# Kernel optimization log

Hardware: AMD Instinct MI355X
Metric: run time of the kernel (lower is better)

## Reference

```python
import jax, jax.numpy as jnp
import numpy as np

EMBED = 256
HEADS = 8
LEVELS = 4
POINTS = 4
HD = EMBED // HEADS  # 32


def _bilinear_sample(v, grid):
    """torch.F.grid_sample(mode='bilinear', padding_mode='zeros', align_corners=False).
    v: (B, C, H, W); grid: (B, Q, P, 2) with xy coords in [-1, 1].
    Returns (B, C, Q, P).
    """
    B, C, H, W = v.shape
    x = (grid[..., 0] + 1.0) * (W * 0.5) - 0.5
    y = (grid[..., 1] + 1.0) * (H * 0.5) - 0.5
    x0f = jnp.floor(x)
    y0f = jnp.floor(y)
    wx = x - x0f
    wy = y - y0f
    x0 = x0f.astype(jnp.int32)
    y0 = y0f.astype(jnp.int32)
    vf = v.reshape(B, C, H * W)

    def corner(xi, yi, w):
        valid = (xi >= 0) & (xi < W) & (yi >= 0) & (yi < H)
        idx = jnp.clip(yi, 0, H - 1) * W + jnp.clip(xi, 0, W - 1)  # (B, Q, P)
        g = jax.vmap(lambda vb, ib: jnp.take(vb, ib, axis=1))(vf, idx.reshape(B, -1))
        g = g.reshape(B, C, idx.shape[1], idx.shape[2])  # (B, C, Q, P)
        return g * (w * valid.astype(v.dtype))[:, None]

    return (corner(x0, y0, (1 - wx) * (1 - wy))
            + corner(x0 + 1, y0, wx * (1 - wy))
            + corner(x0, y0 + 1, (1 - wx) * wy)
            + corner(x0 + 1, y0 + 1, wx * wy))


def setup_inputs() -> dict:
    key = jax.random.key(0)
    ks = jax.random.split(key, 16)
    N, Q, D = 2, 8192, EMBED
    inp = {
        'query': jax.random.normal(ks[0], (N, Q, D), jnp.float32),
        'feat0': jax.random.normal(ks[1], (N, D, 64, 64), jnp.float32),
        'feat1': jax.random.normal(ks[2], (N, D, 32, 32), jnp.float32),
        'feat2': jax.random.normal(ks[3], (N, D, 16, 16), jnp.float32),
        'feat3': jax.random.normal(ks[4], (N, D, 8, 8), jnp.float32),
        'reference_points': jax.random.uniform(ks[5], (N, Q, 2), jnp.float32),
        # params stored as (in, out); equivalent math to torch Linear's x @ W.T + b
        'W_off': jax.random.normal(ks[6], (D, HEADS * LEVELS * POINTS * 2), jnp.float32) * 0.01,
        'b_off': jax.random.normal(ks[7], (HEADS * LEVELS * POINTS * 2,), jnp.float32) * 0.01,
        'W_attn': jax.random.normal(ks[8], (D, HEADS * LEVELS * POINTS), jnp.float32) * 0.02,
        'b_attn': jax.random.normal(ks[9], (HEADS * LEVELS * POINTS,), jnp.float32) * 0.02,
        'W_val': jax.random.normal(ks[10], (D, D), jnp.float32) * (1.0 / np.sqrt(D)),
        'b_val': jnp.zeros((D,), jnp.float32),
        'W_out': jax.random.normal(ks[11], (D, D), jnp.float32) * (1.0 / np.sqrt(D)),
        'b_out': jnp.zeros((D,), jnp.float32),
    }
    return inp


def reference(query, feat0, feat1, feat2, feat3, reference_points,
              W_off, b_off, W_attn, b_attn, W_val, b_val, W_out, b_out):
    feats = [feat0, feat1, feat2, feat3]
    N, Q, D = query.shape
    # offset / attention-weight projections
    off = (query @ W_off + b_off).reshape(N, Q, HEADS, LEVELS, POINTS, 2)
    attn = (query @ W_attn + b_attn).reshape(N, Q, HEADS, LEVELS, POINTS)
    # reference points (N,Q,2) -> (N,Q,L,2)
    ref = jnp.broadcast_to(reference_points[:, :, None, :], (N, Q, LEVELS, 2))
    # value projection (1x1 conv) per level, split heads -> (N*H, hd, H_l, W_l)
    vals = [(jnp.einsum('bchw,cd->bdhw', f, W_val) + b_val[None, :, None, None])
            .reshape(N * HEADS, HD, f.shape[2], f.shape[3]) for f in feats]
    # flatten batch*heads
    off = off.transpose(0, 2, 1, 3, 4, 5).reshape(N * HEADS, Q, LEVELS, POINTS, 2)
    attn = attn.transpose(0, 2, 1, 3, 4).reshape(N * HEADS, Q, LEVELS, POINTS)
    refh = jnp.broadcast_to(ref[:, None], (N, HEADS, Q, LEVELS, 2)).reshape(N * HEADS, Q, LEVELS, 2)
    loc = refh[:, :, :, None, :] + off                 # (NH, Q, L, P, 2) in [0,1]
    grid = 2.0 * loc - 1.0                             # [-1, 1]
    # per-level bilinear sampling -> (NH, hd, Q, L, P)
    sampled = jnp.stack([_bilinear_sample(vals[l], grid[:, :, l]) for l in range(LEVELS)], axis=-2)
    # softmax over levels*points
    aw = jax.nn.softmax(attn.reshape(N * HEADS, Q, LEVELS * POINTS), axis=-1)
    aw = jnp.nan_to_num(aw).reshape(N * HEADS, Q, LEVELS, POINTS)
    out = jnp.einsum('bcqlp,bqlp->bcq', sampled, aw)   # (NH, hd, Q)
    out = out.reshape(N, HEADS, HD, Q).transpose(0, 3, 1, 2).reshape(N, Q, D)
    return out @ W_out + b_out
```

## Files before the change

kernel.cpp:

```cpp
#include <hip/hip_runtime.h>
#include <math.h>

#define NB 2
#define QN 8192
#define DIM 256
#define S_TOT 5440

typedef unsigned int uint32;
typedef _Float16 f16;
typedef __attribute__((ext_vector_type(8))) _Float16 h8;
typedef __attribute__((ext_vector_type(2))) _Float16 h2;
typedef __attribute__((ext_vector_type(4))) float f32x4;
typedef __attribute__((ext_vector_type(4))) uint32 u32x4;

__global__ __launch_bounds__(256) void prep_kernel(
    const float* __restrict__ f0, const float* __restrict__ f1,
    const float* __restrict__ f2, const float* __restrict__ f3,
    const float* __restrict__ W_off, const float* __restrict__ W_attn,
    const float* __restrict__ W_val, const float* __restrict__ W_out,
    f16* __restrict__ featT, f16* __restrict__ Wcat_t,
    f16* __restrict__ Wval_t, f16* __restrict__ Wout_t) {
  const int t = blockIdx.x;
  const float* src;
  f16* dst;
  int S, tb;
  if (t < 340) {
    const int b = (t >= 170) ? 1 : 0;
    const int tt = t - 170 * b;
    int soff;
    if (tt < 128)      { src = f0; S = 4096; soff = 0;    tb = tt; }
    else if (tt < 160) { src = f1; S = 1024; soff = 4096; tb = tt - 128; }
    else if (tt < 168) { src = f2; S = 256;  soff = 5120; tb = tt - 160; }
    else               { src = f3; S = 64;   soff = 5376; tb = tt - 168; }
    src += (size_t)b * 256 * S;
    dst = featT + ((size_t)b * S_TOT + soff) * 256;
  } else {
    const int tw = t - 340;
    if (tw < 8)       { src = W_off;  dst = Wcat_t;             S = 256; tb = tw; }
    else if (tw < 12) { src = W_attn; dst = Wcat_t + 256 * 256; S = 128; tb = tw - 8; }
    else if (tw < 20) { src = W_val;  dst = Wval_t;             S = 256; tb = tw - 12; }
    else              { src = W_out;  dst = Wout_t;             S = 256; tb = tw - 20; }
  }
  const int s0 = tb * 32, c0 = blockIdx.y * 32;

  __shared__ float tile[32][33];
  const int tx = threadIdx.x & 31, ty = threadIdx.x >> 5;
#pragma unroll
  for (int j = 0; j < 4; ++j) {
    const int c = c0 + ty + j * 8;
    tile[ty + j * 8][tx] = src[(size_t)c * S + s0 + tx];
  }
  __syncthreads();
#pragma unroll
  for (int j = 0; j < 4; ++j) {
    const int srow = s0 + ty + j * 8;
    dst[(size_t)srow * 256 + c0 + tx] = (f16)tile[tx][ty + j * 8];
  }
}

__global__ __launch_bounds__(256) void gemm_fused_kernel(
    const f16* __restrict__ featT, const float* __restrict__ query,
    const f16* __restrict__ Wval_t, const f16* __restrict__ Wcat_t,
    const float* __restrict__ b_val, const float* __restrict__ b_off,
    const float* __restrict__ b_attn,
    f16* __restrict__ vals, f16* __restrict__ offb, f16* __restrict__ attnb) {
  __shared__ f16 As[64][256];
  __shared__ f16 Bs[64][256];
  const int t = blockIdx.x;
  const int tid = threadIdx.x;
  const bool isval = (t < 680);
  size_t r0, c0;
  const f16* Bt;
  if (isval) { r0 = (size_t)(t >> 2) * 64;      c0 = (size_t)(t & 3) * 64;  Bt = Wval_t; }
  else       { const int t2 = t - 680;
               r0 = (size_t)(t2 / 6) * 64;      c0 = (size_t)(t2 % 6) * 64; Bt = Wcat_t; }

  {
    const f16* gb = Bt + c0 * 256;
    const int row = tid >> 5, slot = tid & 31;
#pragma unroll
    for (int i = 0; i < 8; ++i) {
      const int r = i * 8 + row;
      const int ph = (slot & 24) | ((slot ^ r) & 7);
      if (isval) {
        *(u32x4*)&As[r][ph * 8] =
            *(const u32x4*)(featT + (r0 + r) * 256 + slot * 8);
      } else {
        const float* ga = query + (r0 + r) * 256 + slot * 8;
        const float4 u0 = *(const float4*)ga;
        const float4 u1 = *(const float4*)(ga + 4);
        h8 hv = {(f16)u0.x, (f16)u0.y, (f16)u0.z, (f16)u0.w,
                 (f16)u1.x, (f16)u1.y, (f16)u1.z, (f16)u1.w};
        *(h8*)&As[r][ph * 8] = hv;
      }
      *(u32x4*)&Bs[r][ph * 8] = *(const u32x4*)(gb + (size_t)r * 256 + slot * 8);
    }
  }
  __syncthreads();

  const int wid = tid >> 6, lane = tid & 63;
  const int wr = (wid >> 1) * 32, wc = (wid & 1) * 32;
  const int l15 = lane & 15, l4 = lane >> 4;

  f32x4 acc[2][2] = {};
#pragma unroll
  for (int ks = 0; ks < 8; ++ks) {
    const int slot = ks * 4 + l4;
    h8 a[2], b[2];
#pragma unroll
    for (int m = 0; m < 2; ++m) {
      const int r = wr + m * 16 + l15;
      const int ph = (slot & 24) | ((slot ^ r) & 7);
      a[m] = *(const h8*)&As[r][ph * 8];
    }
#pragma unroll
    for (int n = 0; n < 2; ++n) {
      const int r = wc + n * 16 + l15;
      const int ph = (slot & 24) | ((slot ^ r) & 7);
      b[n] = *(const h8*)&Bs[r][ph * 8];
    }
#pragma unroll
    for (int m = 0; m < 2; ++m)
#pragma unroll
      for (int n = 0; n < 2; ++n)
        acc[m][n] = __builtin_amdgcn_mfma_f32_16x16x32_f16(a[m], b[n], acc[m][n], 0, 0, 0);
  }

#pragma unroll
  for (int m = 0; m < 2; ++m)
#pragma unroll
    for (int n = 0; n < 2; ++n)
#pragma unroll
      for (int r = 0; r < 4; ++r) {
        const size_t row = r0 + wr + m * 16 + l4 * 4 + r;
        const size_t col = c0 + wc + n * 16 + l15;
        const float v = acc[m][n][r];
        if (isval) {
          vals[row * 256 + col] = (f16)(v + b_val[col]);
        } else if (c0 < 256) {
          offb[row * 256 + col] = (f16)(v + b_off[col]);
        } else {
          attnb[row * 128 + (col - 256)] = (f16)(v + b_attn[col - 256]);
        }
      }
}

__global__ __launch_bounds__(256) void gemm_out_kernel(
    const f16* __restrict__ A, const f16* __restrict__ Bt,
    const float* __restrict__ bias, float* __restrict__ out) {
  __shared__ f16 As[64][256];
  __shared__ f16 Bs[64][256];
  const int tid = threadIdx.x;
  const size_t r0 = (size_t)blockIdx.x * 64;
  const size_t c0 = (size_t)blockIdx.y * 64;

  {
    const f16* ga = A + r0 * 256;
    const f16* gb = Bt + c0 * 256;
    const int row = tid >> 5, slot = tid & 31;
#pragma unroll
    for (int i = 0; i < 8; ++i) {
      const int r = i * 8 + row;
      const int ph = (slot & 24) | ((slot ^ r) & 7);
      *(u32x4*)&As[r][ph * 8] = *(const u32x4*)(ga + (size_t)r * 256 + slot * 8);
      *(u32x4*)&Bs[r][ph * 8] = *(const u32x4*)(gb + (size_t)r * 256 + slot * 8);
    }
  }
  __syncthreads();

  const int wid = tid >> 6, lane = tid & 63;
  const int wr = (wid >> 1) * 32, wc = (wid & 1) * 32;
  const int l15 = lane & 15, l4 = lane >> 4;

  f32x4 acc[2][2] = {};
#pragma unroll
  for (int ks = 0; ks < 8; ++ks) {
    const int slot = ks * 4 + l4;
    h8 a[2], b[2];
#pragma unroll
    for (int m = 0; m < 2; ++m) {
      const int r = wr + m * 16 + l15;
      const int ph = (slot & 24) | ((slot ^ r) & 7);
      a[m] = *(const h8*)&As[r][ph * 8];
    }
#pragma unroll
    for (int n = 0; n < 2; ++n) {
      const int r = wc + n * 16 + l15;
      const int ph = (slot & 24) | ((slot ^ r) & 7);
      b[n] = *(const h8*)&Bs[r][ph * 8];
    }
#pragma unroll
    for (int m = 0; m < 2; ++m)
#pragma unroll
      for (int n = 0; n < 2; ++n)
        acc[m][n] = __builtin_amdgcn_mfma_f32_16x16x32_f16(a[m], b[n], acc[m][n], 0, 0, 0);
  }

#pragma unroll
  for (int m = 0; m < 2; ++m)
#pragma unroll
    for (int n = 0; n < 2; ++n)
#pragma unroll
      for (int r = 0; r < 4; ++r) {
        const size_t row = r0 + wr + m * 16 + l4 * 4 + r;
        const size_t col = c0 + wc + n * 16 + l15;
        out[row * 256 + col] = acc[m][n][r] + bias[col];
      }
}

__global__ __launch_bounds__(256) void sample_kernel(
    const f16* __restrict__ vals, const f16* __restrict__ offb,
    const f16* __restrict__ attnb, const float* __restrict__ refp,
    f16* __restrict__ samp) {
  const int tid = threadIdx.x;
  const int g = tid & 15;
  const int grp = tid >> 4;
  const int h = grp & 7;
  const int half = tid >> 7;
  const int bq = blockIdx.x * 2 + half;
  const int b = bq >> 13;

  __shared__ float4 wts[16][17];
  __shared__ int4 idxs[16][17];

  const float rx = refp[(size_t)bq * 2 + 0];
  const float ry = refp[(size_t)bq * 2 + 1];

  float logit = (float)attnb[(size_t)bq * 128 + h * 16 + g];
  float m = logit;
#pragma unroll
  for (int mask = 1; mask < 16; mask <<= 1)
    m = fmaxf(m, __shfl_xor(m, mask, 16));
  const float e = __expf(logit - m);
  float ssum = e;
#pragma unroll
  for (int mask = 1; mask < 16; mask <<= 1)
    ssum += __shfl_xor(ssum, mask, 16);
  const float aw = e / ssum;

  const h2 ov = *(const h2*)(offb + (size_t)bq * 256 + h * 32 + g * 2);
  const int l = g >> 2;
  const int Wl = 64 >> l;
  const int loff = (l == 0) ? 0 : (l == 1) ? 4096 : (l == 2) ? 5120 : 5376;

  const float px = (rx + (float)ov[0]) * (float)Wl - 0.5f;
  const float py = (ry + (float)ov[1]) * (float)Wl - 0.5f;
  const float fx = floorf(px), fy = floorf(py);
  const float wx = px - fx, wy = py - fy;
  const int x0 = (int)fx, y0 = (int)fy;
  const int x1 = x0 + 1, y1 = y0 + 1;
  const float vx0 = (x0 >= 0 && x0 < Wl) ? 1.f : 0.f;
  const float vx1 = (x1 >= 0 && x1 < Wl) ? 1.f : 0.f;
  const float vy0 = (y0 >= 0 && y0 < Wl) ? 1.f : 0.f;
  const float vy1 = (y1 >= 0 && y1 < Wl) ? 1.f : 0.f;
  const int cx0 = min(max(x0, 0), Wl - 1), cx1 = min(max(x1, 0), Wl - 1);
  const int cy0 = min(max(y0, 0), Wl - 1), cy1 = min(max(y1, 0), Wl - 1);
  const int base = b * S_TOT + loff;
  idxs[grp][g] = make_int4((base + cy0 * Wl + cx0) * 512,
                           (base + cy0 * Wl + cx1) * 512,
                           (base + cy1 * Wl + cx0) * 512,
                           (base + cy1 * Wl + cx1) * 512);
  wts[grp][g] = make_float4(aw * (1.f - wx) * (1.f - wy) * vx0 * vy0,
                            aw * wx * (1.f - wy) * vx1 * vy0,
                            aw * (1.f - wx) * wy * vx0 * vy1,
                            aw * wx * wy * vx1 * vy1);
  __syncthreads();

  const int c4 = g & 3, pc = g >> 2;
  const char* vb = (const char*)vals + (h * 64 + c4 * 16);

  float wv[16];
  int ids[16];
#pragma unroll
  for (int pt = 0; pt < 16; ++pt) {
    wv[pt] = ((const float*)&wts[grp][pt])[pc];
    ids[pt] = ((const int*)&idxs[grp][pt])[pc];
  }
  h8 vv[16];
#pragma unroll
  for (int pt = 0; pt < 16; ++pt) vv[pt] = *(const h8*)(vb + ids[pt]);

  float a[8] = {};
#pragma unroll
  for (int pt = 0; pt < 16; ++pt) {
#pragma unroll
    for (int k = 0; k < 8; ++k) a[k] = fmaf((float)vv[pt][k], wv[pt], a[k]);
  }
#pragma unroll
  for (int k = 0; k < 8; ++k) {
    a[k] += __shfl_xor(a[k], 4);
    a[k] += __shfl_xor(a[k], 8);
  }
  if (pc == 0) {
    h8 r;
#pragma unroll
    for (int k = 0; k < 8; ++k) r[k] = (f16)a[k];
    *(h8*)(samp + (size_t)bq * 256 + h * 32 + c4 * 8) = r;
  }
}

extern "C" void kernel_launch(void* const* d_in, const int* in_sizes, int n_in,
                              void* d_out, int out_size, void* d_ws, size_t ws_size,
                              hipStream_t stream) {
  const float* query = (const float*)d_in[0];
  const float* feat[4] = {(const float*)d_in[1], (const float*)d_in[2],
                          (const float*)d_in[3], (const float*)d_in[4]};
  const float* refp  = (const float*)d_in[5];
  const float* W_off = (const float*)d_in[6];
  const float* b_off = (const float*)d_in[7];
  const float* W_attn = (const float*)d_in[8];
  const float* b_attn = (const float*)d_in[9];
  const float* W_val = (const float*)d_in[10];
  const float* b_val = (const float*)d_in[11];
  const float* W_out = (const float*)d_in[12];
  const float* b_out = (const float*)d_in[13];
  float* out = (float*)d_out;

  f16* ws = (f16*)d_ws;
  f16* featT  = ws;
  f16* vals   = featT + (size_t)NB * S_TOT * 256;
  f16* offb   = vals + (size_t)NB * S_TOT * 256;
  f16* samp   = offb + (size_t)NB * QN * 256;
  f16* attnb  = samp + (size_t)NB * QN * 256;
  f16* Wcat_t = attnb + (size_t)NB * QN * 128;
  f16* Wval_t = Wcat_t + 384 * 256;
  f16* Wout_t = Wval_t + 256 * 256;

  prep_kernel<<<dim3(368, 8), 256, 0, stream>>>(
      feat[0], feat[1], feat[2], feat[3], W_off, W_attn, W_val, W_out,
      featT, Wcat_t, Wval_t, Wout_t);

  gemm_fused_kernel<<<680 + 1536, 256, 0, stream>>>(
      featT, query, Wval_t, Wcat_t, b_val, b_off, b_attn, vals, offb, attnb);

  sample_kernel<<<(NB * QN) / 2, 256, 0, stream>>>(vals, offb, attnb, refp, samp);

  gemm_out_kernel<<<dim3((NB * QN) / 64, 4), 256, 0, stream>>>(
      samp, Wout_t, b_out, out);
}
```

Before: 80.98 us.

## Loop over column tiles per block reusing A tile with B register prefetch

Both GEMM kernels now assign one 64-row strip per block and iterate over all 64-column output tiles. The A tile is loaded (and for query, converted to fp16) once and cached in registers, and the next B tile is prefetched into registers while the current one is used. This removes redundant A loads and conversions across column-tile blocks. In exchange it cuts the grid size by 4-6x, reducing parallelism and raising register pressure.

```diff
diff --git a/kernel.cpp b/kernel.cpp
--- a/kernel.cpp
+++ b/kernel.cpp
@@ -68,81 +68,103 @@
   __shared__ f16 Bs[64][256];
   const int t = blockIdx.x;
   const int tid = threadIdx.x;
-  const bool isval = (t < 680);
-  size_t r0, c0;
-  const f16* Bt;
-  if (isval) { r0 = (size_t)(t >> 2) * 64;      c0 = (size_t)(t & 3) * 64;  Bt = Wval_t; }
-  else       { const int t2 = t - 680;
-               r0 = (size_t)(t2 / 6) * 64;      c0 = (size_t)(t2 % 6) * 64; Bt = Wcat_t; }
-
-  {
-    const f16* gb = Bt + c0 * 256;
-    const int row = tid >> 5, slot = tid & 31;
+  const bool isval = (t < 170);
+  const size_t r0 = (size_t)(isval ? t : t - 170) * 64;
+  const int NC = isval ? 4 : 6;
+  const f16* Bt = isval ? Wval_t : Wcat_t;
+
+  const int row = tid >> 5, slot = tid & 31;
+
+#pragma unroll
+  for (int i = 0; i < 8; ++i) {
+    const int r = i * 8 + row;
+    const int ph = (slot & 24) | ((slot ^ r) & 7);
+    if (isval) {
+      *(u32x4*)&As[r][ph * 8] =
+          *(const u32x4*)(featT + (r0 + r) * 256 + slot * 8);
+    } else {
+      const float* ga = query + (r0 + r) * 256 + slot * 8;
+      const float4 u0 = *(const float4*)ga;
+      const float4 u1 = *(const float4*)(ga + 4);
+      h8 hv = {(f16)u0.x, (f16)u0.y, (f16)u0.z, (f16)u0.w,
+               (f16)u1.x, (f16)u1.y, (f16)u1.z, (f16)u1.w};
+      *(h8*)&As[r][ph * 8] = hv;
+    }
+  }
+
+  const int wid = tid >> 6, lane = tid & 63;
+  const int wr = (wid >> 1) * 32, wc = (wid & 1) * 32;
+  const int l15 = lane & 15, l4 = lane >> 4;
+
+  u32x4 bpre[8];
+#pragma unroll
+  for (int i = 0; i < 8; ++i) {
+    bpre[i] = *(const u32x4*)(Bt + (size_t)(i * 8 + row) * 256 + slot * 8);
+  }
+
+  h8 areg[8][2];
+
+  for (int c = 0; c < NC; ++c) {
+    __syncthreads();
 #pragma unroll
     for (int i = 0; i < 8; ++i) {
       const int r = i * 8 + row;
       const int ph = (slot & 24) | ((slot ^ r) & 7);
-      if (isval) {
-        *(u32x4*)&As[r][ph * 8] =
-            *(const u32x4*)(featT + (r0 + r) * 256 + slot * 8);
-      } else {
-        const float* ga = query + (r0 + r) * 256 + slot * 8;
-        const float4 u0 = *(const float4*)ga;
-        const float4 u1 = *(const float4*)(ga + 4);
-        h8 hv = {(f16)u0.x, (f16)u0.y, (f16)u0.z, (f16)u0.w,
-                 (f16)u1.x, (f16)u1.y, (f16)u1.z, (f16)u1.w};
-        *(h8*)&As[r][ph * 8] = hv;
-      }
-      *(u32x4*)&Bs[r][ph * 8] = *(const u32x4*)(gb + (size_t)r * 256 + slot * 8);
-    }
-  }
-  __syncthreads();
-
-  const int wid = tid >> 6, lane = tid & 63;
-  const int wr = (wid >> 1) * 32, wc = (wid & 1) * 32;
-  const int l15 = lane & 15, l4 = lane >> 4;
-
-  f32x4 acc[2][2] = {};
-#pragma unroll
-  for (int ks = 0; ks < 8; ++ks) {
-    const int slot = ks * 4 + l4;
-    h8 a[2], b[2];
-#pragma unroll
-    for (int m = 0; m < 2; ++m) {
-      const int r = wr + m * 16 + l15;
-      const int ph = (slot & 24) | ((slot ^ r) & 7);
-      a[m] = *(const h8*)&As[r][ph * 8];
-    }
-#pragma unroll
-    for (int n = 0; n < 2; ++n) {
-      const int r = wc + n * 16 + l15;
-      const int ph = (slot & 24) | ((slot ^ r) & 7);
-      b[n] = *(const h8*)&Bs[r][ph * 8];
-    }
+      *(u32x4*)&Bs[r][ph * 8] = bpre[i];
+    }
+    __syncthreads();
+
+    if (c + 1 < NC) {
+#pragma unroll
+      for (int i = 0; i < 8; ++i) {
+        bpre[i] = *(const u32x4*)(Bt + (size_t)((c + 1) * 64 + i * 8 + row) * 256 + slot * 8);
+      }
+    }
+
+    f32x4 acc[2][2] = {};
+#pragma unroll
+    for (int ks = 0; ks < 8; ++ks) {
+      const int slot2 = ks * 4 + l4;
+      if (c == 0) {
+#pragma unroll
+        for (int m = 0; m < 2; ++m) {
+          const int r = wr + m * 16 + l15;
+          const int ph = (slot2 & 24) | ((slot2 ^ r) & 7);
+          areg[ks][m] = *(const h8*)&As[r][ph * 8];
+        }
+      }
+      h8 b[2];
+#pragma unroll
+      for (int n = 0; n < 2; ++n) {
+        const int r = wc + n * 16 + l15;
+        const int ph = (slot2 & 24) | ((slot2 ^ r) & 7);
+        b[n] = *(const h8*)&Bs[r][ph * 8];
+      }
+#pragma unroll
+      for (int m = 0; m < 2; ++m)
+#pragma unroll
+        for (int n = 0; n < 2; ++n)
+          acc[m][n] = __builtin_amdgcn_mfma_f32_16x16x32_f16(areg[ks][m], b[n], acc[m][n], 0, 0, 0);
+    }
+
 #pragma unroll
     for (int m = 0; m < 2; ++m)
 #pragma unroll
       for (int n = 0; n < 2; ++n)
-        acc[m][n] = __builtin_amdgcn_mfma_f32_16x16x32_f16(a[m], b[n], acc[m][n], 0, 0, 0);
-  }
-
-#pragma unroll
-  for (int m = 0; m < 2; ++m)
-#pragma unroll
-    for (int n = 0; n < 2; ++n)
-#pragma unroll
-      for (int r = 0; r < 4; ++r) {
-        const size_t row = r0 + wr + m * 16 + l4 * 4 + r;
-        const size_t col = c0 + wc + n * 16 + l15;
-        const float v = acc[m][n][r];
-        if (isval) {
-          vals[row * 256 + col] = (f16)(v + b_val[col]);
-        } else if (c0 < 256) {
-          offb[row * 256 + col] = (f16)(v + b_off[col]);
-        } else {
-          attnb[row * 128 + (col - 256)] = (f16)(v + b_attn[col - 256]);
+#pragma unroll
+        for (int r = 0; r < 4; ++r) {
+          const size_t rw = r0 + wr + m * 16 + l4 * 4 + r;
+          const int col = c * 64 + wc + n * 16 + l15;
+          const float v = acc[m][n][r];
+          if (isval) {
+            vals[rw * 256 + col] = (f16)(v + b_val[col]);
+          } else if (col < 256) {
+            offb[rw * 256 + col] = (f16)(v + b_off[col]);
+          } else {
+            attnb[rw * 128 + (col - 256)] = (f16)(v + b_attn[col - 256]);
+          }
         }
-      }
+  }
 }
 
 __global__ __launch_bounds__(256) void gemm_out_kernel(
@@ -152,60 +174,81 @@
   __shared__ f16 Bs[64][256];
   const int tid = threadIdx.x;
   const size_t r0 = (size_t)blockIdx.x * 64;
-  const size_t c0 = (size_t)blockIdx.y * 64;
-
-  {
-    const f16* ga = A + r0 * 256;
-    const f16* gb = Bt + c0 * 256;
-    const int row = tid >> 5, slot = tid & 31;
+
+  const int row = tid >> 5, slot = tid & 31;
+#pragma unroll
+  for (int i = 0; i < 8; ++i) {
+    const int r = i * 8 + row;
+    const int ph = (slot & 24) | ((slot ^ r) & 7);
+    *(u32x4*)&As[r][ph * 8] = *(const u32x4*)(A + (r0 + r) * 256 + slot * 8);
+  }
+
+  const int wid = tid >> 6, lane = tid & 63;
+  const int wr = (wid >> 1) * 32, wc = (wid & 1) * 32;
+  const int l15 = lane & 15, l4 = lane >> 4;
+
+  u32x4 bpre[8];
+#pragma unroll
+  for (int i = 0; i < 8; ++i) {
+    bpre[i] = *(const u32x4*)(Bt + (size_t)(i * 8 + row) * 256 + slot * 8);
+  }
+
+  h8 areg[8][2];
+
+  for (int c = 0; c < 4; ++c) {
+    __syncthreads();
 #pragma unroll
     for (int i = 0; i < 8; ++i) {
       const int r = i * 8 + row;
       const int ph = (slot & 24) | ((slot ^ r) & 7);
-      *(u32x4*)&As[r][ph * 8] = *(const u32x4*)(ga + (size_t)r * 256 + slot * 8);
-      *(u32x4*)&Bs[r][ph * 8] = *(const u32x4*)(gb + (size_t)r * 256 + slot * 8);
-    }
-  }
-  __syncthreads();
-
-  const int wid = tid >> 6, lane = tid & 63;
-  const int wr = (wid >> 1) * 32, wc = (wid & 1) * 32;
-  const int l15 = lane & 15, l4 = lane >> 4;
-
-  f32x4 acc[2][2] = {};
-#pragma unroll
-  for (int ks = 0; ks < 8; ++ks) {
-    const int slot = ks * 4 + l4;
-    h8 a[2], b[2];
-#pragma unroll
-    for (int m = 0; m < 2; ++m) {
-      const int r = wr + m * 16 + l15;
-      const int ph = (slot & 24) | ((slot ^ r) & 7);
-      a[m] = *(const h8*)&As[r][ph * 8];
-    }
-#pragma unroll
-    for (int n = 0; n < 2; ++n) {
-      const int r = wc + n * 16 + l15;
-      const int ph = (slot & 24) | ((slot ^ r) & 7);
-      b[n] = *(const h8*)&Bs[r][ph * 8];
-    }
+      *(u32x4*)&Bs[r][ph * 8] = bpre[i];
+    }
+    __syncthreads();
+
+    if (c + 1 < 4) {
+#pragma unroll
+      for (int i = 0; i < 8; ++i) {
+        bpre[i] = *(const u32x4*)(Bt + (size_t)((c + 1) * 64 + i * 8 + row) * 256 + slot * 8);
+      }
+    }
+
+    f32x4 acc[2][2] = {};
+#pragma unroll
+    for (int ks = 0; ks < 8; ++ks) {
+      const int slot2 = ks * 4 + l4;
+      if (c == 0) {
+#pragma unroll
+        for (int m = 0; m < 2; ++m) {
+          const int r = wr + m * 16 + l15;
+          const int ph = (slot2 & 24) | ((slot2 ^ r) & 7);
+          areg[ks][m] = *(const h8*)&As[r][ph * 8];
+        }
+      }
+      h8 b[2];
+#pragma unroll
+      for (int n = 0; n < 2; ++n) {
+        const int r = wc + n * 16 + l15;
+        const int ph = (slot2 & 24) | ((slot2 ^ r) & 7);
+        b[n] = *(const h8*)&Bs[r][ph * 8];
+      }
+#pragma unroll
+      for (int m = 0; m < 2; ++m)
+#pragma unroll
+        for (int n = 0; n < 2; ++n)
+          acc[m][n] = __builtin_amdgcn_mfma_f32_16x16x32_f16(areg[ks][m], b[n], acc[m][n], 0, 0, 0);
+    }
+
 #pragma unroll
     for (int m = 0; m < 2; ++m)
 #pragma unroll
       for (int n = 0; n < 2; ++n)
-        acc[m][n] = __builtin_amdgcn_mfma_f32_16x16x32_f16(a[m], b[n], acc[m][n], 0, 0, 0);
-  }
-
-#pragma unroll
-  for (int m = 0; m < 2; ++m)
-#pragma unroll
-    for (int n = 0; n < 2; ++n)
-#pragma unroll
-      for (int r = 0; r < 4; ++r) {
-        const size_t row = r0 + wr + m * 16 + l4 * 4 + r;
-        const size_t col = c0 + wc + n * 16 + l15;
-        out[row * 256 + col] = acc[m][n][r] + bias[col];
-      }
+#pragma unroll
+        for (int r = 0; r < 4; ++r) {
+          const size_t rw = r0 + wr + m * 16 + l4 * 4 + r;
+          const int col = c * 64 + wc + n * 16 + l15;
+          out[rw * 256 + col] = acc[m][n][r] + bias[col];
+        }
+  }
 }
 
 __global__ __launch_bounds__(256) void sample_kernel(
@@ -330,11 +373,10 @@
       feat[0], feat[1], feat[2], feat[3], W_off, W_attn, W_val, W_out,
       featT, Wcat_t, Wval_t, Wout_t);
 
-  gemm_fused_kernel<<<680 + 1536, 256, 0, stream>>>(
+  gemm_fused_kernel<<<170 + 256, 256, 0, stream>>>(
       featT, query, Wval_t, Wcat_t, b_val, b_off, b_attn, vals, offb, attnb);
 
   sample_kernel<<<(NB * QN) / 2, 256, 0, stream>>>(vals, offb, attnb, refp, samp);
 
-  gemm_out_kernel<<<dim3((NB * QN) / 64, 4), 256, 0, stream>>>(
-      samp, Wout_t, b_out, out);
-}
+  gemm_out_kernel<<<(NB * QN) / 64, 256, 0, stream>>>(samp, Wout_t, b_out, out);
+}
```

Measured after the change: 69.28 us. 14.5% less time.

## Pre-swizzle GEMM operands into MFMA fragment layout and drop LDS staging

Applied to the files above, without the earlier changes.

Query, features, weights and sampled outputs are written by the producers in a blocked fragment layout (16-row groups × 8-wide K chunks), so the GEMM kernels load MFMA operands straight from global memory without shared-memory staging or barriers. Query fp32→fp16 conversion moves into the prep kernel. GEMM tiles change to 32 rows × full width per block, so each block covers all output columns and there are fewer, larger blocks. The intent is to remove LDS traffic and syncs. In exchange, weight fragments are re-read from global/L2 by every block and the query conversion becomes an extra pass through memory. The samp buffer is aliased onto qf to reuse workspace.

```diff
diff --git a/kernel.cpp b/kernel.cpp
--- a/kernel.cpp
+++ b/kernel.cpp
@@ -11,207 +11,198 @@
 typedef __attribute__((ext_vector_type(8))) _Float16 h8;
 typedef __attribute__((ext_vector_type(2))) _Float16 h2;
 typedef __attribute__((ext_vector_type(4))) float f32x4;
-typedef __attribute__((ext_vector_type(4))) uint32 u32x4;
+
 
 __global__ __launch_bounds__(256) void prep_kernel(
+    const float* __restrict__ q,
     const float* __restrict__ f0, const float* __restrict__ f1,
     const float* __restrict__ f2, const float* __restrict__ f3,
     const float* __restrict__ W_off, const float* __restrict__ W_attn,
     const float* __restrict__ W_val, const float* __restrict__ W_out,
-    f16* __restrict__ featT, f16* __restrict__ Wcat_t,
-    f16* __restrict__ Wval_t, f16* __restrict__ Wout_t) {
-  const int t = blockIdx.x;
+    f16* __restrict__ qf, f16* __restrict__ featT_f,
+    f16* __restrict__ Wcat_f, f16* __restrict__ Wval_f, f16* __restrict__ Wout_f) {
+  const int t = blockIdx.x, y = blockIdx.y, tid = threadIdx.x;
+
+  if (t < 128) {
+    const int row0 = (t * 8 + y) * 16;
+    const int s_l = tid >> 4, c8 = tid & 15;
+    const float* src = q + (size_t)(row0 + s_l) * 256;
+#pragma unroll
+    for (int cc = 0; cc < 2; ++cc) {
+      const int c8c = c8 + cc * 16;
+      const float4 u0 = *(const float4*)(src + c8c * 8);
+      const float4 u1 = *(const float4*)(src + c8c * 8 + 4);
+      h8 hv = {(f16)u0.x, (f16)u0.y, (f16)u0.z, (f16)u0.w,
+               (f16)u1.x, (f16)u1.y, (f16)u1.z, (f16)u1.w};
+      *(h8*)(qf + ((size_t)(row0 >> 4) * 32 + c8c) * 128 + s_l * 8) = hv;
+    }
+    return;
+  }
+
+  __shared__ float tile[32][33];
+  const int tx = tid & 31, ty = tid >> 5;
   const float* src;
   f16* dst;
-  int S, tb;
-  if (t < 340) {
-    const int b = (t >= 170) ? 1 : 0;
-    const int tt = t - 170 * b;
+  int S, tb, s_base = 0;
+
+  if (t < 468) {
+    const int tt0 = t - 128;
+    const int b = (tt0 >= 170) ? 1 : 0;
+    const int tt = tt0 - 170 * b;
     int soff;
     if (tt < 128)      { src = f0; S = 4096; soff = 0;    tb = tt; }
     else if (tt < 160) { src = f1; S = 1024; soff = 4096; tb = tt - 128; }
     else if (tt < 168) { src = f2; S = 256;  soff = 5120; tb = tt - 160; }
     else               { src = f3; S = 64;   soff = 5376; tb = tt - 168; }
     src += (size_t)b * 256 * S;
-    dst = featT + ((size_t)b * S_TOT + soff) * 256;
+    dst = featT_f;
+    s_base = b * S_TOT + soff;
   } else {
-    const int tw = t - 340;
-    if (tw < 8)       { src = W_off;  dst = Wcat_t;             S = 256; tb = tw; }
-    else if (tw < 12) { src = W_attn; dst = Wcat_t + 256 * 256; S = 128; tb = tw - 8; }
-    else if (tw < 20) { src = W_val;  dst = Wval_t;             S = 256; tb = tw - 12; }
-    else              { src = W_out;  dst = Wout_t;             S = 256; tb = tw - 20; }
-  }
-  const int s0 = tb * 32, c0 = blockIdx.y * 32;
-
-  __shared__ float tile[32][33];
-  const int tx = threadIdx.x & 31, ty = threadIdx.x >> 5;
+    const int tw = t - 468;
+    if (tw < 8)       { src = W_off;  dst = Wcat_f; S = 256; tb = tw;      s_base = 0; }
+    else if (tw < 12) { src = W_attn; dst = Wcat_f; S = 128; tb = tw - 8;  s_base = 256; }
+    else if (tw < 20) { src = W_val;  dst = Wval_f; S = 256; tb = tw - 12; s_base = 0; }
+    else              { src = W_out;  dst = Wout_f; S = 256; tb = tw - 20; s_base = 0; }
+  }
+  const int s0 = tb * 32, c0 = y * 32;
+
 #pragma unroll
   for (int j = 0; j < 4; ++j) {
     const int c = c0 + ty + j * 8;
     tile[ty + j * 8][tx] = src[(size_t)c * S + s0 + tx];
   }
   __syncthreads();
-#pragma unroll
-  for (int j = 0; j < 4; ++j) {
-    const int srow = s0 + ty + j * 8;
-    dst[(size_t)srow * 256 + c0 + tx] = (f16)tile[tx][ty + j * 8];
+
+  if (tid < 128) {
+    const int s_l = tid >> 2, c8l = tid & 3;
+    const int Sg = s_base + s0 + s_l;
+    const int c8 = (c0 >> 3) + c8l;
+    h8 v;
+#pragma unroll
+    for (int j = 0; j < 8; ++j) v[j] = (f16)tile[c8l * 8 + j][s_l];
+    *(h8*)(dst + ((size_t)(Sg >> 4) * 32 + c8) * 128 + (Sg & 15) * 8) = v;
   }
 }
 
 __global__ __launch_bounds__(256) void gemm_fused_kernel(
-    const f16* __restrict__ featT, const float* __restrict__ query,
-    const f16* __restrict__ Wval_t, const f16* __restrict__ Wcat_t,
+    const f16* __restrict__ qf, const f16* __restrict__ featT_f,
+    const f16* __restrict__ Wcat_f, const f16* __restrict__ Wval_f,
     const float* __restrict__ b_val, const float* __restrict__ b_off,
     const float* __restrict__ b_attn,
     f16* __restrict__ vals, f16* __restrict__ offb, f16* __restrict__ attnb) {
-  __shared__ f16 As[64][256];
-  __shared__ f16 Bs[64][256];
   const int t = blockIdx.x;
   const int tid = threadIdx.x;
-  const bool isval = (t < 680);
-  size_t r0, c0;
-  const f16* Bt;
-  if (isval) { r0 = (size_t)(t >> 2) * 64;      c0 = (size_t)(t & 3) * 64;  Bt = Wval_t; }
-  else       { const int t2 = t - 680;
-               r0 = (size_t)(t2 / 6) * 64;      c0 = (size_t)(t2 % 6) * 64; Bt = Wcat_t; }
-
-  {
-    const f16* gb = Bt + c0 * 256;
-    const int row = tid >> 5, slot = tid & 31;
-#pragma unroll
-    for (int i = 0; i < 8; ++i) {
-      const int r = i * 8 + row;
-      const int ph = (slot & 24) | ((slot ^ r) & 7);
-      if (isval) {
-        *(u32x4*)&As[r][ph * 8] =
-            *(const u32x4*)(featT + (r0 + r) * 256 + slot * 8);
-      } else {
-        const float* ga = query + (r0 + r) * 256 + slot * 8;
-        const float4 u0 = *(const float4*)ga;
-        const float4 u1 = *(const float4*)(ga + 4);
-        h8 hv = {(f16)u0.x, (f16)u0.y, (f16)u0.z, (f16)u0.w,
-                 (f16)u1.x, (f16)u1.y, (f16)u1.z, (f16)u1.w};
-        *(h8*)&As[r][ph * 8] = hv;
-      }
-      *(u32x4*)&Bs[r][ph * 8] = *(const u32x4*)(gb + (size_t)r * 256 + slot * 8);
+  const int lane = tid & 63, wid = tid >> 6;
+  const int l15 = lane & 15, l4 = lane >> 4;
+
+  if (t < 340) {
+    const int g0 = t * 2;
+    f32x4 acc[2][4] = {};
+#pragma unroll
+    for (int ks = 0; ks < 8; ++ks) {
+      const int s2 = ks * 4 + l4;
+      h8 a[2], b[4];
+#pragma unroll
+      for (int m = 0; m < 2; ++m)
+        a[m] = *(const h8*)(featT_f + ((size_t)(g0 + m) * 32 + s2) * 128 + l15 * 8);
+#pragma unroll
+      for (int n = 0; n < 4; ++n)
+        b[n] = *(const h8*)(Wval_f + ((size_t)(wid * 4 + n) * 32 + s2) * 128 + l15 * 8);
+#pragma unroll
+      for (int m = 0; m < 2; ++m)
+#pragma unroll
+        for (int n = 0; n < 4; ++n)
+          acc[m][n] = __builtin_amdgcn_mfma_f32_16x16x32_f16(a[m], b[n], acc[m][n], 0, 0, 0);
     }
-  }
-  __syncthreads();
-
-  const int wid = tid >> 6, lane = tid & 63;
-  const int wr = (wid >> 1) * 32, wc = (wid & 1) * 32;
-  const int l15 = lane & 15, l4 = lane >> 4;
-
-  f32x4 acc[2][2] = {};
-#pragma unroll
-  for (int ks = 0; ks < 8; ++ks) {
-    const int slot = ks * 4 + l4;
-    h8 a[2], b[2];
-#pragma unroll
-    for (int m = 0; m < 2; ++m) {
-      const int r = wr + m * 16 + l15;
-      const int ph = (slot & 24) | ((slot ^ r) & 7);
-      a[m] = *(const h8*)&As[r][ph * 8];
+#pragma unroll
+    for (int m = 0; m < 2; ++m)
+#pragma unroll
+      for (int n = 0; n < 4; ++n)
+#pragma unroll
+        for (int r = 0; r < 4; ++r) {
+          const size_t rw = (size_t)t * 32 + m * 16 + l4 * 4 + r;
+          const int col = wid * 64 + n * 16 + l15;
+          vals[rw * 256 + col] = (f16)(acc[m][n][r] + b_val[col]);
+        }
+  } else {
+    const int t2 = t - 340;
+    const int g0 = t2 * 2;
+    f32x4 acc[2][6] = {};
+#pragma unroll
+    for (int ks = 0; ks < 8; ++ks) {
+      const int s2 = ks * 4 + l4;
+      h8 a[2], b[6];
+#pragma unroll
+      for (int m = 0; m < 2; ++m)
+        a[m] = *(const h8*)(qf + ((size_t)(g0 + m) * 32 + s2) * 128 + l15 * 8);
+#pragma unroll
+      for (int n = 0; n < 6; ++n)
+        b[n] = *(const h8*)(Wcat_f + ((size_t)(wid * 6 + n) * 32 + s2) * 128 + l15 * 8);
+#pragma unroll
+      for (int m = 0; m < 2; ++m)
+#pragma unroll
+        for (int n = 0; n < 6; ++n)
+          acc[m][n] = __builtin_amdgcn_mfma_f32_16x16x32_f16(a[m], b[n], acc[m][n], 0, 0, 0);
     }
 #pragma unroll
-    for (int n = 0; n < 2; ++n) {
-      const int r = wc + n * 16 + l15;
-      const int ph = (slot & 24) | ((slot ^ r) & 7);
-      b[n] = *(const h8*)&Bs[r][ph * 8];
-    }
-#pragma unroll
     for (int m = 0; m < 2; ++m)
 #pragma unroll
-      for (int n = 0; n < 2; ++n)
-        acc[m][n] = __builtin_amdgcn_mfma_f32_16x16x32_f16(a[m], b[n], acc[m][n], 0, 0, 0);
-  }
-
-#pragma unroll
-  for (int m = 0; m < 2; ++m)
-#pragma unroll
-    for (int n = 0; n < 2; ++n)
-#pragma unroll
-      for (int r = 0; r < 4; ++r) {
-        const size_t row = r0 + wr + m * 16 + l4 * 4 + r;
-        const size_t col = c0 + wc + n * 16 + l15;
-        const float v = acc[m][n][r];
-        if (isval) {
-          vals[row * 256 + col] = (f16)(v + b_val[col]);
-        } else if (c0 < 256) {
-          offb[row * 256 + col] = (f16)(v + b_off[col]);
-        } else {
-          attnb[row * 128 + (col - 256)] = (f16)(v + b_attn[col - 256]);
+      for (int n = 0; n < 6; ++n)
+#pragma unroll
+        for (int r = 0; r < 4; ++r) {
+          const size_t rw = (size_t)t2 * 32 + m * 16 + l4 * 4 + r;
+          const int col = wid * 96 + n * 16 + l15;
+          const float v = acc[m][n][r];
+          if (col < 256)
+            offb[rw * 256 + col] = (f16)(v + b_off[col]);
+          else
+            attnb[rw * 128 + (col - 256)] = (f16)(v + b_attn[col - 256]);
         }
-      }
+  }
 }
 
 __global__ __launch_bounds__(256) void gemm_out_kernel(
     const f16* __restrict__ A, const f16* __restrict__ Bt,
     const float* __restrict__ bias, float* __restrict__ out) {
-  __shared__ f16 As[64][256];
-  __shared__ f16 Bs[64][256];
   const int tid = threadIdx.x;
-  const size_t r0 = (size_t)blockIdx.x * 64;
-  const size_t c0 = (size_t)blockIdx.y * 64;
-
-  {
-    const f16* ga = A + r0 * 256;
-    const f16* gb = Bt + c0 * 256;
-    const int row = tid >> 5, slot = tid & 31;
-#pragma unroll
-    for (int i = 0; i < 8; ++i) {
-      const int r = i * 8 + row;
-      const int ph = (slot & 24) | ((slot ^ r) & 7);
-      *(u32x4*)&As[r][ph * 8] = *(const u32x4*)(ga + (size_t)r * 256 + slot * 8);
-      *(u32x4*)&Bs[r][ph * 8] = *(const u32x4*)(gb + (size_t)r * 256 + slot * 8);
-    }
-  }
-  __syncthreads();
-
-  const int wid = tid >> 6, lane = tid & 63;
-  const int wr = (wid >> 1) * 32, wc = (wid & 1) * 32;
+  const int lane = tid & 63, wid = tid >> 6;
   const int l15 = lane & 15, l4 = lane >> 4;
-
-  f32x4 acc[2][2] = {};
+  const int g0 = blockIdx.x * 2;
+
+  f32x4 acc[2][4] = {};
 #pragma unroll
   for (int ks = 0; ks < 8; ++ks) {
-    const int slot = ks * 4 + l4;
-    h8 a[2], b[2];
-#pragma unroll
-    for (int m = 0; m < 2; ++m) {
-      const int r = wr + m * 16 + l15;
-      const int ph = (slot & 24) | ((slot ^ r) & 7);
-      a[m] = *(const h8*)&As[r][ph * 8];
-    }
-#pragma unroll
-    for (int n = 0; n < 2; ++n) {
-      const int r = wc + n * 16 + l15;
-      const int ph = (slot & 24) | ((slot ^ r) & 7);
-      b[n] = *(const h8*)&Bs[r][ph * 8];
-    }
+    const int s2 = ks * 4 + l4;
+    h8 a[2], b[4];
 #pragma unroll
     for (int m = 0; m < 2; ++m)
-#pragma unroll
-      for (int n = 0; n < 2; ++n)
+      a[m] = *(const h8*)(A + ((size_t)(g0 + m) * 32 + s2) * 128 + l15 * 8);
+#pragma unroll
+    for (int n = 0; n < 4; ++n)
+      b[n] = *(const h8*)(Bt + ((size_t)(wid * 4 + n) * 32 + s2) * 128 + l15 * 8);
+#pragma unroll
+    for (int m = 0; m < 2; ++m)
+#pragma unroll
+      for (int n = 0; n < 4; ++n)
         acc[m][n] = __builtin_amdgcn_mfma_f32_16x16x32_f16(a[m], b[n], acc[m][n], 0, 0, 0);
   }
 
 #pragma unroll
   for (int m = 0; m < 2; ++m)
 #pragma unroll
-    for (int n = 0; n < 2; ++n)
+    for (int n = 0; n < 4; ++n)
 #pragma unroll
       for (int r = 0; r < 4; ++r) {
-        const size_t row = r0 + wr + m * 16 + l4 * 4 + r;
-        const size_t col = c0 + wc + n * 16 + l15;
-        out[row * 256 + col] = acc[m][n][r] + bias[col];
+        const size_t rw = (size_t)blockIdx.x * 32 + m * 16 + l4 * 4 + r;
+        const int col = wid * 64 + n * 16 + l15;
+        out[rw * 256 + col] = acc[m][n][r] + bias[col];
       }
 }
 
 __global__ __launch_bounds__(256) void sample_kernel(
     const f16* __restrict__ vals, const f16* __restrict__ offb,
     const f16* __restrict__ attnb, const float* __restrict__ refp,
-    f16* __restrict__ samp) {
+    f16* __restrict__ samp_f) {
   const int tid = threadIdx.x;
   const int g = tid & 15;
   const int grp = tid >> 4;
@@ -295,7 +286,7 @@
     h8 r;
 #pragma unroll
     for (int k = 0; k < 8; ++k) r[k] = (f16)a[k];
-    *(h8*)(samp + (size_t)bq * 256 + h * 32 + c4 * 8) = r;
+    *(h8*)(samp_f + ((size_t)(bq >> 4) * 32 + h * 4 + c4) * 128 + (bq & 15) * 8) = r;
   }
 }
 
@@ -317,24 +308,24 @@
   float* out = (float*)d_out;
 
   f16* ws = (f16*)d_ws;
-  f16* featT  = ws;
-  f16* vals   = featT + (size_t)NB * S_TOT * 256;
-  f16* offb   = vals + (size_t)NB * S_TOT * 256;
-  f16* samp   = offb + (size_t)NB * QN * 256;
-  f16* attnb  = samp + (size_t)NB * QN * 256;
-  f16* Wcat_t = attnb + (size_t)NB * QN * 128;
-  f16* Wval_t = Wcat_t + 384 * 256;
-  f16* Wout_t = Wval_t + 256 * 256;
-
-  prep_kernel<<<dim3(368, 8), 256, 0, stream>>>(
-      feat[0], feat[1], feat[2], feat[3], W_off, W_attn, W_val, W_out,
-      featT, Wcat_t, Wval_t, Wout_t);
-
-  gemm_fused_kernel<<<680 + 1536, 256, 0, stream>>>(
-      featT, query, Wval_t, Wcat_t, b_val, b_off, b_attn, vals, offb, attnb);
-
-  sample_kernel<<<(NB * QN) / 2, 256, 0, stream>>>(vals, offb, attnb, refp, samp);
-
-  gemm_out_kernel<<<dim3((NB * QN) / 64, 4), 256, 0, stream>>>(
-      samp, Wout_t, b_out, out);
-}
+  f16* vals    = ws;
+  f16* offb    = vals + (size_t)NB * S_TOT * 256;
+  f16* attnb   = offb + (size_t)NB * QN * 256;
+  f16* qf      = attnb + (size_t)NB * QN * 128;
+  f16* samp_f  = qf;
+  f16* featT_f = qf + (size_t)NB * QN * 256;
+  f16* Wcat_f  = featT_f + (size_t)NB * S_TOT * 256;
+  f16* Wval_f  = Wcat_f + 384 * 256;
+  f16* Wout_f  = Wval_f + 256 * 256;
+
+  prep_kernel<<<dim3(496, 8), 256, 0, stream>>>(
+      query, feat[0], feat[1], feat[2], feat[3],
+      W_off, W_attn, W_val, W_out, qf, featT_f, Wcat_f, Wval_f, Wout_f);
+
+  gemm_fused_kernel<<<340 + 512, 256, 0, stream>>>(
+      qf, featT_f, Wcat_f, Wval_f, b_val, b_off, b_attn, vals, offb, attnb);
+
+  sample_kernel<<<(NB * QN) / 2, 256, 0, stream>>>(vals, offb, attnb, refp, samp_f);
+
+  gemm_out_kernel<<<(NB * QN) / 32, 256, 0, stream>>>(samp_f, Wout_f, b_out, out);
+}
```

After: 69.34 us. 14.4% less time.
